# Kernel tuning notes

Measured on AMD Instinct MI355X. Metric: run time of the kernel, lower is better.

Reference implementation:

```python
import jax, jax.numpy as jnp
import numpy as np

WINDOW = 14

def _make_rel_index(ws):
    coords = np.stack(np.meshgrid(np.arange(ws), np.arange(ws), indexing='ij'))  # [2,ws,ws]
    flat = coords.reshape(2, -1)
    rel = flat[:, :, None] - flat[:, None, :]            # [2,N,N]
    rel = rel.transpose(1, 2, 0).copy()
    rel[:, :, 0] += ws - 1
    rel[:, :, 1] += ws - 1
    rel[:, :, 0] *= 2 * ws - 1
    return rel.sum(-1).astype(np.int32)                  # [N,N]

def setup_inputs() -> dict:
    key = jax.random.key(0)
    ks = jax.random.split(key, 7)
    B, N, C, H = 256, WINDOW * WINDOW, 768, 12
    s = 0.02
    return {
        'x': jax.random.normal(ks[0], (B, N, C), jnp.float32),
        'qkv_w': jax.random.normal(ks[1], (3 * C, C), jnp.float32) * s,
        'q_bias': jnp.zeros((C,), jnp.float32),
        'v_bias': jnp.zeros((C,), jnp.float32),
        'rpb_table': jax.random.normal(ks[2], ((2 * WINDOW - 1) ** 2, H), jnp.float32) * s,
        'proj_w': jax.random.normal(ks[3], (C, C), jnp.float32) * s,
        'proj_b': jnp.zeros((C,), jnp.float32),
        'rel_index': jnp.asarray(_make_rel_index(WINDOW)),
        'num_heads': H,
    }

def reference(x, qkv_w, q_bias, v_bias, rpb_table, proj_w, proj_b, rel_index, num_heads):
    B, N, C = x.shape
    H = num_heads
    hd = C // H
    scale = hd ** -0.5
    qkv_bias = jnp.concatenate([q_bias, jnp.zeros_like(v_bias), v_bias])
    qkv = x @ qkv_w.T + qkv_bias                          # [B,N,3C]
    qkv = qkv.reshape(B, N, 3, H, hd).transpose(2, 0, 3, 1, 4)  # [3,B,H,N,hd]
    q, k, v = qkv[0] * scale, qkv[1], qkv[2]
    attn = jnp.einsum('bhnd,bhmd->bhnm', q, k)            # [B,H,N,N]
    rpb = rpb_table[rel_index.reshape(-1)].reshape(N, N, H).transpose(2, 0, 1)  # [H,N,N]
    attn = jax.nn.softmax(attn + rpb, axis=-1)
    out = jnp.einsum('bhnm,bhmd->bhnd', attn, v)          # [B,H,N,hd]
    out = out.transpose(0, 2, 1, 3).reshape(B, N, C)
    return out @ proj_w.T + proj_b
```

## Files before the change

kernel.cpp:

```cpp
#include <hip/hip_runtime.h>
#include <hip/hip_fp16.h>

typedef _Float16 f16;
typedef __attribute__((ext_vector_type(8))) _Float16 f16x8;
typedef __attribute__((ext_vector_type(4))) float f32x4;

#define MFMA16 __builtin_amdgcn_mfma_f32_16x16x32_f16
#define BAR() __builtin_amdgcn_s_barrier()
#define VMCNT(n) asm volatile("s_waitcnt vmcnt(" #n ")" ::: "memory")
#define LGKM(n) asm volatile("s_waitcnt lgkmcnt(" #n ")" ::: "memory")
#define SCHEDB() __builtin_amdgcn_sched_barrier(0)

__device__ __forceinline__ void gload16(const f16* g, char* l) {
  __builtin_amdgcn_global_load_lds(
      (const __attribute__((address_space(1))) void*)g,
      (__attribute__((address_space(3))) void*)l, 16, 0, 0);
}

__global__ __launch_bounds__(256) void cvt_k(const float* __restrict__ in,
                                             f16* __restrict__ out, int n8) {
  int i = blockIdx.x * 256 + threadIdx.x;
  const int stride = gridDim.x * 256;
  for (; i < n8; i += stride) {
    const float4* p = (const float4*)(in + (size_t)i * 8);
    float4 a = p[0], b = p[1];
    f16x8 h;
    h[0] = (f16)a.x; h[1] = (f16)a.y; h[2] = (f16)a.z; h[3] = (f16)a.w;
    h[4] = (f16)b.x; h[5] = (f16)b.y; h[6] = (f16)b.z; h[7] = (f16)b.w;
    *(f16x8*)(out + (size_t)i * 8) = h;
  }
}

__global__ __launch_bounds__(256) void rpb_build_k(const float* __restrict__ tab,
                                                   const int* __restrict__ rel,
                                                   f16* __restrict__ out) {
  int i = blockIdx.x * 256 + threadIdx.x;
  if (i >= 196 * 196) return;
  int idx = rel[i];
#pragma unroll
  for (int h = 0; h < 12; ++h)
    out[h * (196 * 196) + i] = (f16)tab[idx * 12 + h];
}

template <int MODE>
__global__ __launch_bounds__(512) void gemm_k(
    const f16* __restrict__ A, const f16* __restrict__ W,
    const float* __restrict__ bias_a, const float* __restrict__ bias_b,
    f16* __restrict__ q_out, f16* __restrict__ k_out, f16* __restrict__ vT_out,
    float* __restrict__ f_out) {
  constexpr int NTIL = (MODE == 0) ? 9 : 3;
  constexpr int NWG = (MODE == 0) ? 1764 : 588;
  constexpr int QX = NWG / 8, RX = NWG % 8;
  constexpr int KT = 12;

  extern __shared__ char lds[];

  const int tid = threadIdx.x;
  const int lane = tid & 63, wid = tid >> 6;
  const int xcd = blockIdx.x & 7, bix = blockIdx.x >> 3;
  const int lbid =
      (xcd < RX ? xcd * (QX + 1) : RX * (QX + 1) + (xcd - RX) * QX) + bix;
  const int brow = lbid / NTIL, bcol = lbid % NTIL;
  const int wr = wid >> 2, wc = wid & 3;
  const int l15 = lane & 15, g4 = lane >> 4;

  const int sr = wid * 8 + (lane >> 3);
  const int scw = ((lane & 7) ^ (lane >> 3)) * 8;
  const f16* pAt = A + (size_t)(brow * 256 + sr) * 768 + scw;
  const f16* pBt = W + (size_t)(bcol * 256 + sr) * 768 + scw;
  char* ldsW = lds + wid * 1024;

  auto stA = [&](int kt, int hf, int buf) {
#pragma unroll
    for (int i = 0; i < 2; ++i)
      gload16(pAt + (size_t)(hf * 128 + i * 64) * 768 + kt * 64,
              ldsW + buf * 65536 + hf * 16384 + i * 8192);
  };
  auto stB = [&](int kt, int hf, int buf) {
#pragma unroll
    for (int i = 0; i < 2; ++i)
      gload16(pBt + (size_t)(hf * 128 + i * 64) * 768 + kt * 64,
              ldsW + buf * 65536 + 32768 + hf * 16384 + i * 8192);
  };

  f16x8 af[2][4][2], bf[2][2][2];
  const int aswz = l15 & 7;
  const char* ldsAl = lds + (size_t)(wr * 128 + l15) * 128;
  const char* ldsBl = lds + 32768 + (size_t)(wc * 64 + l15) * 128;

  auto rdA = [&](int q, int buf) {
#pragma unroll
    for (int mf = 0; mf < 4; ++mf)
#pragma unroll
      for (int ks = 0; ks < 2; ++ks)
        af[q][mf][ks] = *(const f16x8*)(ldsAl + buf * 65536 +
                                        (q * 64 + mf * 16) * 128 +
                                        ((ks * 4 + g4) ^ aswz) * 16);
  };
  auto rdB = [&](int r, int buf) {
#pragma unroll
    for (int nf = 0; nf < 2; ++nf)
#pragma unroll
      for (int ks = 0; ks < 2; ++ks)
        bf[r][nf][ks] = *(const f16x8*)(ldsBl + buf * 65536 +
                                        (r * 32 + nf * 16) * 128 +
                                        ((ks * 4 + g4) ^ aswz) * 16);
  };

  const f32x4 zero4 = {0.f, 0.f, 0.f, 0.f};
  f32x4 acc[8][4];
#pragma unroll
  for (int i = 0; i < 8; ++i)
#pragma unroll
    for (int j = 0; j < 4; ++j) acc[i][j] = zero4;

  auto mm = [&](int q, int r) {
#pragma unroll
    for (int ks = 0; ks < 2; ++ks)
#pragma unroll
      for (int mf = 0; mf < 4; ++mf)
#pragma unroll
        for (int nf = 0; nf < 2; ++nf)
          acc[q * 4 + mf][r * 2 + nf] =
              MFMA16(af[q][mf][ks], bf[r][nf][ks], acc[q * 4 + mf][r * 2 + nf],
                     0, 0, 0);
  };

  stA(0, 0, 0); stA(0, 1, 0); stB(0, 0, 0); stB(0, 1, 0);
  stA(1, 0, 1); stA(1, 1, 1);
  VMCNT(4);
  BAR();

  for (int t = 0; t < KT; ++t) {
    const int cur = t & 1, nxt = cur ^ 1;
    rdA(0, cur); rdB(0, cur);
    if (t + 1 < KT) stB(t + 1, 0, nxt);
    LGKM(8);
    BAR(); LGKM(0); SCHEDB();
    __builtin_amdgcn_s_setprio(1); mm(0, 0); __builtin_amdgcn_s_setprio(0);
    BAR();
    rdA(1, cur);
    if (t + 1 < KT) stB(t + 1, 1, nxt);
    BAR(); LGKM(0); SCHEDB();
    __builtin_amdgcn_s_setprio(1); mm(1, 0); __builtin_amdgcn_s_setprio(0);
    BAR();
    rdB(1, cur);
    if (t + 2 < KT) stA(t + 2, 0, cur);
    BAR(); LGKM(0); SCHEDB();
    __builtin_amdgcn_s_setprio(1); mm(0, 1); __builtin_amdgcn_s_setprio(0);
    BAR();
    if (t + 2 < KT) stA(t + 2, 1, cur);
    if (t < KT - 2) { VMCNT(4); } else if (t == KT - 2) { VMCNT(0); }
    BAR(); SCHEDB();
    __builtin_amdgcn_s_setprio(1); mm(1, 1); __builtin_amdgcn_s_setprio(0);
    BAR();
  }

#pragma unroll
  for (int mf = 0; mf < 8; ++mf) {
    const int rowo = wr * 128 + (mf >> 2) * 64 + (mf & 3) * 16 + g4 * 4;
#pragma unroll
    for (int rr = 0; rr < 4; ++rr) {
      const int grow = brow * 256 + rowo + rr;
      if constexpr (MODE == 0) {
        const int bI = grow / 196;
        const int nI = grow - bI * 196;
#pragma unroll
        for (int nf = 0; nf < 4; ++nf) {
          const int col = bcol * 256 + wc * 64 + (nf >> 1) * 32 + (nf & 1) * 16 + l15;
          const int s = bcol / 3;
          const int rem = col - s * 768;
          const int hh = rem >> 6, dd = rem & 63;
          float v = acc[mf][nf][rr];
          if (s == 0) {
            v = (v + bias_a[rem]) * 0.125f;
            q_out[(((size_t)bI * 12 + hh) * 196 + nI) * 64 + dd] = (f16)v;
          } else if (s == 1) {
            k_out[(((size_t)bI * 12 + hh) * 196 + nI) * 64 + dd] = (f16)v;
          } else {
            v += bias_b[rem];
            vT_out[(((size_t)bI * 12 + hh) * 64 + dd) * 224 + nI] = (f16)v;
          }
        }
      } else {
        float* orow = f_out + (size_t)grow * 768;
#pragma unroll
        for (int nf = 0; nf < 4; ++nf) {
          const int col = bcol * 256 + wc * 64 + (nf >> 1) * 32 + (nf & 1) * 16 + l15;
          orow[col] = acc[mf][nf][rr] + bias_a[col];
        }
      }
    }
  }
}

__global__ __launch_bounds__(256) void attn_k(const f16* __restrict__ qg,
                                              const f16* __restrict__ kg,
                                              const f16* __restrict__ vTg,
                                              const f16* __restrict__ rpb,
                                              f16* __restrict__ og) {
  extern __shared__ char smem[];
  f16x8* Klds = (f16x8*)smem;
  f16x8* Vlds = (f16x8*)(smem + 26624);
  f16x8* Plds = (f16x8*)(smem + 59392);

  const int tid = threadIdx.x;
  const int bh = blockIdx.x;
  const int b = bh / 12, h = bh - b * 12;
  const int lane = tid & 63, wid = tid >> 6;
  const int l15 = lane & 15, g4 = lane >> 4;

  f16x8 z8;
#pragma unroll
  for (int j = 0; j < 8; ++j) z8[j] = (f16)0.f;

  const f16* kgb = kg + (size_t)bh * (196 * 64);
  for (int c = tid; c < 196 * 8; c += 256) {
    int m = c >> 3, dc = c & 7;
    Klds[m * 8 + (dc ^ (m & 7))] = *(const f16x8*)(kgb + m * 64 + dc * 8);
  }
  const f16* vgb = vTg + (size_t)bh * (64 * 224);
  for (int c = tid; c < 64 * 32; c += 256) {
    int d = c >> 5, mc = c & 31;
    f16x8 v;
    if (mc < 24) {
      v = *(const f16x8*)(vgb + d * 224 + mc * 8);
    } else if (mc == 24) {
      v = *(const f16x8*)(vgb + d * 224 + mc * 8);
#pragma unroll
      for (int j = 4; j < 8; ++j) v[j] = (f16)0.f;
    } else {
      v = z8;
    }
    Vlds[d * 32 + (mc ^ (d & 7))] = v;
  }
  f16x8* Pw = Plds + wid * (16 * 32);
  if (g4 < 2) {
    int n = l15;
    Pw[n * 32 + ((26 + g4) ^ (n & 7))] = z8;
  }
  __syncthreads();

  const f16* qgb = qg + (size_t)bh * (196 * 64);
  const f16* rpbh = rpb + (size_t)h * (196 * 196);

  for (int rt = wid; rt < 13; rt += 4) {
    const int n0 = rt * 16;
    f16x8 qf0 = *(const f16x8*)(qgb + (n0 + l15) * 64 + g4 * 8);
    f16x8 qf1 = *(const f16x8*)(qgb + (n0 + l15) * 64 + 32 + g4 * 8);

    float rv[13][4];
#pragma unroll
    for (int mt = 0; mt < 13; ++mt) {
      const int m = mt * 16 + l15;
      const int mcl = (m < 196) ? m : 195;
#pragma unroll
      for (int r = 0; r < 4; ++r) {
        const int n = n0 + g4 * 4 + r;
        const int ncl = (n < 196) ? n : 195;
        rv[mt][r] = (float)rpbh[ncl * 196 + mcl];
      }
    }

    const f32x4 zero4 = {0.f, 0.f, 0.f, 0.f};
    f32x4 s[13];
#pragma unroll
    for (int mt = 0; mt < 13; ++mt) {
      const int m = mt * 16 + l15;
      f16x8 k0 = Klds[m * 8 + ((g4) ^ (m & 7))];
      f16x8 k1 = Klds[m * 8 + ((4 + g4) ^ (m & 7))];
      s[mt] = MFMA16(qf0, k0, zero4, 0, 0, 0);
      s[mt] = MFMA16(qf1, k1, s[mt], 0, 0, 0);
    }

    float mx[4] = {-3e38f, -3e38f, -3e38f, -3e38f};
#pragma unroll
    for (int mt = 0; mt < 13; ++mt) {
      const int m = mt * 16 + l15;
#pragma unroll
      for (int r = 0; r < 4; ++r) {
        const int n = n0 + g4 * 4 + r;
        float v = (m < 196 && n < 196) ? s[mt][r] + rv[mt][r] : -1e30f;
        s[mt][r] = v;
        mx[r] = fmaxf(mx[r], v);
      }
    }
#pragma unroll
    for (int r = 0; r < 4; ++r) {
      mx[r] = fmaxf(mx[r], __shfl_xor(mx[r], 1));
      mx[r] = fmaxf(mx[r], __shfl_xor(mx[r], 2));
      mx[r] = fmaxf(mx[r], __shfl_xor(mx[r], 4));
      mx[r] = fmaxf(mx[r], __shfl_xor(mx[r], 8));
    }
    float sm[4] = {0.f, 0.f, 0.f, 0.f};
#pragma unroll
    for (int mt = 0; mt < 13; ++mt)
#pragma unroll
      for (int r = 0; r < 4; ++r) {
        float p = __expf(s[mt][r] - mx[r]);
        s[mt][r] = p;
        sm[r] += p;
      }
#pragma unroll
    for (int r = 0; r < 4; ++r) {
      sm[r] += __shfl_xor(sm[r], 1);
      sm[r] += __shfl_xor(sm[r], 2);
      sm[r] += __shfl_xor(sm[r], 4);
      sm[r] += __shfl_xor(sm[r], 8);
    }
    float rinv[4];
#pragma unroll
    for (int r = 0; r < 4; ++r) rinv[r] = 1.f / sm[r];

#pragma unroll
    for (int mt = 0; mt < 13; ++mt) {
      const int m = mt * 16 + l15;
#pragma unroll
      for (int r = 0; r < 4; ++r) {
        const int n = g4 * 4 + r;
        f16* dst = (f16*)Pw + n * 256 + (((m >> 3) ^ (n & 7)) << 3) + (m & 7);
        *dst = (f16)s[mt][r];
      }
    }

    f32x4 o[4];
#pragma unroll
    for (int dt = 0; dt < 4; ++dt) o[dt] = zero4;
#pragma unroll
    for (int ks = 0; ks < 7; ++ks) {
      f16x8 pa = Pw[l15 * 32 + ((ks * 4 + g4) ^ (l15 & 7))];
#pragma unroll
      for (int dt = 0; dt < 4; ++dt) {
        const int d = dt * 16 + l15;
        f16x8 vf = Vlds[d * 32 + ((ks * 4 + g4) ^ (d & 7))];
        o[dt] = MFMA16(pa, vf, o[dt], 0, 0, 0);
      }
    }

#pragma unroll
    for (int r = 0; r < 4; ++r) {
      const int n = n0 + g4 * 4 + r;
      if (n < 196) {
        f16* orow = og + ((size_t)b * 196 + n) * 768 + h * 64;
#pragma unroll
        for (int dt = 0; dt < 4; ++dt)
          orow[dt * 16 + l15] = (f16)(o[dt][r] * rinv[r]);
      }
    }
  }
}

extern "C" void kernel_launch(void* const* d_in, const int* in_sizes, int n_in,
                              void* d_out, int out_size, void* d_ws, size_t ws_size,
                              hipStream_t stream) {
  const float* x = (const float*)d_in[0];
  const float* qkv_w = (const float*)d_in[1];
  const float* q_bias = (const float*)d_in[2];
  const float* v_bias = (const float*)d_in[3];
  const float* rpb_tab = (const float*)d_in[4];
  const float* proj_w = (const float*)d_in[5];
  const float* proj_b = (const float*)d_in[6];
  const int* rel = (const int*)d_in[7];
  float* out = (float*)d_out;

  const size_t SZ_Q = 77070336;
  const size_t SZ_K = 77070336;
  const size_t SZ_VT = 88080384;
  const size_t SZ_AO = 77070336;
  const size_t SZ_RP = 921984;
  const size_t SZ_WQ = 3538944;
  const size_t SZ_WP = 1179648;
  if (ws_size < SZ_Q + SZ_K + SZ_VT + SZ_AO + SZ_RP + SZ_WQ + SZ_WP) return;

  char* w = (char*)d_ws;
  f16* q_ = (f16*)w;
  f16* k_ = (f16*)(w + SZ_Q);
  f16* vT_ = (f16*)(w + SZ_Q + SZ_K);
  f16* ao_ = (f16*)(w + SZ_Q + SZ_K + SZ_VT);
  f16* rp_ = (f16*)(w + SZ_Q + SZ_K + SZ_VT + SZ_AO);
  f16* whq_ = (f16*)(w + SZ_Q + SZ_K + SZ_VT + SZ_AO + SZ_RP);
  f16* whp_ = (f16*)(w + SZ_Q + SZ_K + SZ_VT + SZ_AO + SZ_RP + SZ_WQ);
  f16* xh_ = ao_;

  (void)hipFuncSetAttribute((const void*)attn_k,
                            hipFuncAttributeMaxDynamicSharedMemorySize, 92160);
  (void)hipFuncSetAttribute((const void*)gemm_k<0>,
                            hipFuncAttributeMaxDynamicSharedMemorySize, 131072);
  (void)hipFuncSetAttribute((const void*)gemm_k<1>,
                            hipFuncAttributeMaxDynamicSharedMemorySize, 131072);

  cvt_k<<<2048, 256, 0, stream>>>(x, xh_, 50176 * 768 / 8);
  cvt_k<<<864, 256, 0, stream>>>(qkv_w, whq_, 2304 * 768 / 8);
  cvt_k<<<288, 256, 0, stream>>>(proj_w, whp_, 768 * 768 / 8);
  rpb_build_k<<<(196 * 196 + 255) / 256, 256, 0, stream>>>(rpb_tab, rel, rp_);

  gemm_k<0><<<1764, 512, 131072, stream>>>(xh_, whq_, q_bias, v_bias,
                                           q_, k_, vT_, nullptr);
  attn_k<<<3072, 256, 92160, stream>>>(q_, k_, vT_, rp_, ao_);
  gemm_k<1><<<588, 512, 131072, stream>>>(ao_, whp_, proj_b, nullptr,
                                          nullptr, nullptr, nullptr, out);
}
```

Before: 778.3 us.

## Simplify GEMM pipeline to single-stage prefetch; read K from global in attention

The GEMM main loop swaps its interleaved multi-barrier schedule, which prefetched A two steps ahead, for a simpler double-buffer. Each iteration issues all next-tile global-to-LDS loads up front, then does all LDS reads and MFMAs with a single barrier. The attention kernel stops staging K in shared memory and reads K fragments straight from global memory, cutting LDS from 92160 to 65536 bytes. The aims are fewer barriers in the GEMM and higher occupancy in attention. The risks are less load latency hiding in the GEMM and repeated, uncoalesced global K reads across waves.

```diff
diff --git a/kernel.cpp b/kernel.cpp
--- a/kernel.cpp
+++ b/kernel.cpp
@@ -49,7 +49,7 @@
     f16* __restrict__ q_out, f16* __restrict__ k_out, f16* __restrict__ vT_out,
     float* __restrict__ f_out) {
   constexpr int NTIL = (MODE == 0) ? 9 : 3;
-  constexpr int NWG = (MODE == 0) ? 1764 : 588;
+  constexpr int NWG = 196 * NTIL;
   constexpr int QX = NWG / 8, RX = NWG % 8;
   constexpr int KT = 12;
 
@@ -127,32 +127,25 @@
   };
 
   stA(0, 0, 0); stA(0, 1, 0); stB(0, 0, 0); stB(0, 1, 0);
-  stA(1, 0, 1); stA(1, 1, 1);
-  VMCNT(4);
+  VMCNT(0);
   BAR();
 
   for (int t = 0; t < KT; ++t) {
     const int cur = t & 1, nxt = cur ^ 1;
+    if (t + 1 < KT) {
+      stA(t + 1, 0, nxt); stA(t + 1, 1, nxt);
+      stB(t + 1, 0, nxt); stB(t + 1, 1, nxt);
+    }
     rdA(0, cur); rdB(0, cur);
-    if (t + 1 < KT) stB(t + 1, 0, nxt);
-    LGKM(8);
-    BAR(); LGKM(0); SCHEDB();
-    __builtin_amdgcn_s_setprio(1); mm(0, 0); __builtin_amdgcn_s_setprio(0);
-    BAR();
-    rdA(1, cur);
-    if (t + 1 < KT) stB(t + 1, 1, nxt);
-    BAR(); LGKM(0); SCHEDB();
-    __builtin_amdgcn_s_setprio(1); mm(1, 0); __builtin_amdgcn_s_setprio(0);
-    BAR();
-    rdB(1, cur);
-    if (t + 2 < KT) stA(t + 2, 0, cur);
-    BAR(); LGKM(0); SCHEDB();
-    __builtin_amdgcn_s_setprio(1); mm(0, 1); __builtin_amdgcn_s_setprio(0);
-    BAR();
-    if (t + 2 < KT) stA(t + 2, 1, cur);
-    if (t < KT - 2) { VMCNT(4); } else if (t == KT - 2) { VMCNT(0); }
-    BAR(); SCHEDB();
-    __builtin_amdgcn_s_setprio(1); mm(1, 1); __builtin_amdgcn_s_setprio(0);
+    SCHEDB();
+    rdA(1, cur); rdB(1, cur);
+    LGKM(12);
+    SCHEDB();
+    __builtin_amdgcn_s_setprio(1); mm(0, 0); mm(0, 1); __builtin_amdgcn_s_setprio(0);
+    LGKM(0);
+    SCHEDB();
+    __builtin_amdgcn_s_setprio(1); mm(1, 0); mm(1, 1); __builtin_amdgcn_s_setprio(0);
+    VMCNT(0);
     BAR();
   }
 
@@ -200,9 +193,8 @@
                                               const f16* __restrict__ rpb,
                                               f16* __restrict__ og) {
   extern __shared__ char smem[];
-  f16x8* Klds = (f16x8*)smem;
-  f16x8* Vlds = (f16x8*)(smem + 26624);
-  f16x8* Plds = (f16x8*)(smem + 59392);
+  f16x8* Vlds = (f16x8*)smem;
+  f16x8* Plds = (f16x8*)(smem + 32768);
 
   const int tid = threadIdx.x;
   const int bh = blockIdx.x;
@@ -214,11 +206,6 @@
 #pragma unroll
   for (int j = 0; j < 8; ++j) z8[j] = (f16)0.f;
 
-  const f16* kgb = kg + (size_t)bh * (196 * 64);
-  for (int c = tid; c < 196 * 8; c += 256) {
-    int m = c >> 3, dc = c & 7;
-    Klds[m * 8 + (dc ^ (m & 7))] = *(const f16x8*)(kgb + m * 64 + dc * 8);
-  }
   const f16* vgb = vTg + (size_t)bh * (64 * 224);
   for (int c = tid; c < 64 * 32; c += 256) {
     int d = c >> 5, mc = c & 31;
@@ -242,6 +229,7 @@
   __syncthreads();
 
   const f16* qgb = qg + (size_t)bh * (196 * 64);
+  const f16* kgb = kg + (size_t)bh * (196 * 64);
   const f16* rpbh = rpb + (size_t)h * (196 * 196);
 
   for (int rt = wid; rt < 13; rt += 4) {
@@ -267,8 +255,8 @@
 #pragma unroll
     for (int mt = 0; mt < 13; ++mt) {
       const int m = mt * 16 + l15;
-      f16x8 k0 = Klds[m * 8 + ((g4) ^ (m & 7))];
-      f16x8 k1 = Klds[m * 8 + ((4 + g4) ^ (m & 7))];
+      f16x8 k0 = *(const f16x8*)(kgb + m * 64 + g4 * 8);
+      f16x8 k1 = *(const f16x8*)(kgb + m * 64 + 32 + g4 * 8);
       s[mt] = MFMA16(qf0, k0, zero4, 0, 0, 0);
       s[mt] = MFMA16(qf1, k1, s[mt], 0, 0, 0);
     }
@@ -383,7 +371,7 @@
   f16* xh_ = ao_;
 
   (void)hipFuncSetAttribute((const void*)attn_k,
-                            hipFuncAttributeMaxDynamicSharedMemorySize, 92160);
+                            hipFuncAttributeMaxDynamicSharedMemorySize, 65536);
   (void)hipFuncSetAttribute((const void*)gemm_k<0>,
                             hipFuncAttributeMaxDynamicSharedMemorySize, 131072);
   (void)hipFuncSetAttribute((const void*)gemm_k<1>,
@@ -396,7 +384,7 @@
 
   gemm_k<0><<<1764, 512, 131072, stream>>>(xh_, whq_, q_bias, v_bias,
                                            q_, k_, vT_, nullptr);
-  attn_k<<<3072, 256, 92160, stream>>>(q_, k_, vT_, rp_, ao_);
+  attn_k<<<3072, 256, 65536, stream>>>(q_, k_, vT_, rp_, ao_);
   gemm_k<1><<<588, 512, 131072, stream>>>(ao_, whp_, proj_b, nullptr,
                                           nullptr, nullptr, nullptr, out);
 }
```

Measured after the change: 774.5 us. No clear change (-0.5%).
